# Kernel optimization log

Measured on AMD Instinct MI355X. Metric: run time of the kernel, lower is better.

The kernel has to match this reference:

```python
import jax, jax.numpy as jnp
import numpy as np

N_ITERS = 5
STRICT_MAXIMA_BONUS = 10.0
MAX_SUBPIXEL_SHIFT = 0.6


def setup_inputs() -> dict:
    key = jax.random.key(0)
    return {"x": jax.random.normal(key, (2, 4, 8, 256, 256), dtype=jnp.float32)}


def _nms3d_mask(x):
    # Strict 3x3x3 maxima: x > max over the 26 neighbors, replicate padding
    # (matches kornia nms3d(input, (3,3,3), mask_only=True)).
    B, C, D, H, W = x.shape
    p = jnp.pad(x, ((0, 0), (0, 0), (1, 1), (1, 1), (1, 1)), mode='edge')
    neigh_max = None
    for dd in range(3):
        for dh in range(3):
            for dw in range(3):
                if dd == 1 and dh == 1 and dw == 1:
                    continue
                s = p[:, :, dd:dd + D, dh:dh + H, dw:dw + W]
                neigh_max = s if neigh_max is None else jnp.maximum(neigh_max, s)
    return x > neigh_max


def _solve_cramer_sym3x3(dxx, dyy, dss, dxy, dxs, dys, r0, r1, r2):
    cf00 = dyy * dss - dys * dys
    cf01 = dxy * dss - dys * dxs
    cf02 = dxy * dys - dyy * dxs
    det = dxx * cf00 - dxy * cf01 + dxs * cf02
    solved = jnp.abs(det) > 0.0
    safe_det = jnp.where(solved, det, jnp.ones_like(det))
    sx = (r0 * cf00 - dxy * (r1 * dss - dys * r2) + dxs * (r1 * dys - dyy * r2)) / safe_det
    sy = (dxx * (r1 * dss - dys * r2) - r0 * cf01 + dxs * (dxy * r2 - r1 * dxs)) / safe_det
    ss = (dxx * (dyy * r2 - r1 * dys) - dxy * (dxy * r2 - r1 * dxs) + r0 * cf02) / safe_det
    return sx, sy, ss, solved


def _iterative_quad_interp3d(x, n_iters, strict_maxima_bonus, max_subpixel_shift):
    B, C, D, H, W = x.shape
    dtype = x.dtype
    BC = B * C
    HW = H * W
    DHW = D * HW
    i32 = jnp.int32

    # default grid coordinates, channel order [scale, x, y] as in the torch code
    gd = jnp.broadcast_to(jnp.arange(D, dtype=dtype)[:, None, None], (D, H, W))
    gw = jnp.broadcast_to(jnp.arange(W, dtype=dtype)[None, None, :], (D, H, W))
    gh = jnp.broadcast_to(jnp.arange(H, dtype=dtype)[None, :, None], (D, H, W))
    coords0 = jnp.broadcast_to(jnp.stack([gd, gw, gh], 0)[None, None], (B, C, 3, D, H, W))

    if D < 3 or H < 3 or W < 3:
        return coords0, x

    mask = _nms3d_mask(x)                       # (B,C,D,H,W) strict NMS maxima
    inp = x.reshape(BC, D, H, W)
    flat = inp.reshape(-1)
    m = mask.reshape(BC, D, H, W)

    # dense per-voxel formulation: every voxel runs the keypoint loop; only
    # voxels under the NMS mask are written out at the end (identical math,
    # since each keypoint's iteration depends only on its own patch chain).
    d0 = jnp.broadcast_to(jnp.arange(D, dtype=i32)[None, :, None, None], (BC, D, H, W))
    h0 = jnp.broadcast_to(jnp.arange(H, dtype=i32)[None, None, :, None], (BC, D, H, W))
    w0 = jnp.broadcast_to(jnp.arange(W, dtype=i32)[None, None, None, :], (BC, D, H, W))
    bc_base = (jnp.arange(BC, dtype=i32) * DHW)[:, None, None, None]

    d_cur, h_cur, w_cur = d0, h0, w0
    valid = jnp.ones((BC, D, H, W), dtype=bool)
    zeros = jnp.zeros((BC, D, H, W), dtype=dtype)
    shift_x, shift_y, shift_s, gds = zeros, zeros, zeros, zeros

    for _ in range(n_iters):
        d_s = jnp.clip(d_cur, 1, D - 2)
        h_s = jnp.clip(h_cur, 1, H - 2)
        w_s = jnp.clip(w_cur, 1, W - 2)
        base = bc_base + d_s * HW + h_s * W + w_s

        def tap(od, oh, ow):
            return jnp.take(flat, base + (od * HW + oh * W + ow))

        c000 = tap(0, 0, 0)
        p_xm = tap(0, 0, -1); p_xp = tap(0, 0, 1)
        p_ym = tap(0, -1, 0); p_yp = tap(0, 1, 0)
        p_sm = tap(-1, 0, 0); p_sp = tap(1, 0, 0)

        gx = 0.5 * (p_xp - p_xm)
        gy = 0.5 * (p_yp - p_ym)
        gs = 0.5 * (p_sp - p_sm)
        dxx = p_xp - 2.0 * c000 + p_xm
        dyy = p_yp - 2.0 * c000 + p_ym
        dss = p_sp - 2.0 * c000 + p_sm
        dxy = 0.25 * (tap(0, 1, 1) - tap(0, 1, -1) - tap(0, -1, 1) + tap(0, -1, -1))
        dxs = 0.25 * (tap(1, 0, 1) - tap(1, 0, -1) - tap(-1, 0, 1) + tap(-1, 0, -1))
        dys = 0.25 * (tap(1, 1, 0) - tap(1, -1, 0) - tap(-1, 1, 0) + tap(-1, -1, 0))

        sx, sy, ss, solved = _solve_cramer_sym3x3(dxx, dyy, dss, dxy, dxs, dys, -gx, -gy, -gs)
        valid = valid & solved
        vf = valid.astype(dtype)
        sx = sx * vf; sy = sy * vf; ss = ss * vf
        shift_x = jnp.where(valid, sx, shift_x)
        shift_y = jnp.where(valid, sy, shift_y)
        shift_s = jnp.where(valid, ss, shift_s)
        gds = jnp.where(valid, gx * sx + gy * sy + gs * ss, gds)

        # data-dependent recentering, sequentially per axis (x -> y -> scale)
        mv = (valid & (sx > max_subpixel_shift)).astype(i32) - (valid & (sx < -max_subpixel_shift)).astype(i32)
        new_w = w_cur + mv
        valid = valid & (new_w >= 1) & (new_w <= W - 2)
        w_cur = jnp.clip(new_w, 0, W - 1)

        mv = (valid & (sy > max_subpixel_shift)).astype(i32) - (valid & (sy < -max_subpixel_shift)).astype(i32)
        new_h = h_cur + mv
        valid = valid & (new_h >= 1) & (new_h <= H - 2)
        h_cur = jnp.clip(new_h, 0, H - 1)

        mv = (valid & (ss > max_subpixel_shift)).astype(i32) - (valid & (ss < -max_subpixel_shift)).astype(i32)
        new_d = d_cur + mv
        valid = valid & (new_d >= 1) & (new_d <= D - 2)
        d_cur = jnp.clip(new_d, 0, D - 1)

    valid = valid & (jnp.abs(shift_x) <= 1.5) & (jnp.abs(shift_y) <= 1.5) & (jnp.abs(shift_s) <= 1.5)

    final_s = jnp.where(valid, d_cur.astype(dtype) + shift_s, d0.astype(dtype))
    final_x = jnp.where(valid, w_cur.astype(dtype) + shift_x, w0.astype(dtype))
    final_y = jnp.where(valid, h_cur.astype(dtype) + shift_y, h0.astype(dtype))
    finals = jnp.stack([final_s, final_x, final_y], 1).reshape(B, C, 3, D, H, W)
    coords_max = jnp.where(mask[:, :, None], finals, coords0)

    corr = 0.5 * jnp.where(valid, gds, zeros)
    if strict_maxima_bonus > 0:
        corr = corr + strict_maxima_bonus * valid.astype(dtype)
    y_max = jnp.where(m, inp + corr, inp).reshape(B, C, D, H, W)
    return coords_max, y_max


def reference(x):
    return _iterative_quad_interp3d(x, N_ITERS, STRICT_MAXIMA_BONUS, MAX_SUBPIXEL_SHIFT)
```

## Files before the change

### kernel.cpp

```cpp
#include <hip/hip_runtime.h>

#define WD 256
#define HT 256
#define DP 8
#define NBC 8
#define HW 65536
#define DHW 524288
#define NVOX 4194304

__device__ void refine_write(const float* __restrict__ x,
                             float* __restrict__ out,
                             int idx) {
#pragma clang fp contract(off)
    const int w0 = idx & 255;
    const int h0 = (idx >> 8) & 255;
    const int d0 = (idx >> 16) & 7;
    const int bc = idx >> 19;
    int d = d0, h = h0, w = w0;
    bool valid = true;
    float shx = 0.f, shy = 0.f, shs = 0.f, gds = 0.f;
    const float* xb = x + (size_t)bc * DHW;
    for (int it = 0; it < 5; ++it) {
        int dcl = min(max(d, 1), DP - 2);
        int hcl = min(max(h, 1), HT - 2);
        int wcl = min(max(w, 1), WD - 2);
        const float* q = xb + dcl * HW + hcl * WD + wcl;
        float c000 = q[0];
        float pxm = q[-1],   pxp = q[1];
        float pym = q[-WD],  pyp = q[WD];
        float psm = q[-HW],  psp = q[HW];
        float gx = 0.5f * (pxp - pxm);
        float gy = 0.5f * (pyp - pym);
        float gs = 0.5f * (psp - psm);
        float dxx = pxp - 2.0f * c000 + pxm;
        float dyy = pyp - 2.0f * c000 + pym;
        float dss = psp - 2.0f * c000 + psm;
        float dxy = 0.25f * (q[WD + 1]  - q[WD - 1]  - q[-WD + 1]  + q[-WD - 1]);
        float dxs = 0.25f * (q[HW + 1]  - q[HW - 1]  - q[-HW + 1]  + q[-HW - 1]);
        float dys = 0.25f * (q[HW + WD] - q[HW - WD] - q[-HW + WD] + q[-HW - WD]);
        float r0 = -gx, r1 = -gy, r2 = -gs;
        float cf00 = dyy * dss - dys * dys;
        float cf01 = dxy * dss - dys * dxs;
        float cf02 = dxy * dys - dyy * dxs;
        float det = dxx * cf00 - dxy * cf01 + dxs * cf02;
        bool solved = fabsf(det) > 0.0f;
        float sdet = solved ? det : 1.0f;
        float sx = (r0 * cf00 - dxy * (r1 * dss - dys * r2) + dxs * (r1 * dys - dyy * r2)) / sdet;
        float sy = (dxx * (r1 * dss - dys * r2) - r0 * cf01 + dxs * (dxy * r2 - r1 * dxs)) / sdet;
        float ss = (dxx * (dyy * r2 - r1 * dys) - dxy * (dxy * r2 - r1 * dxs) + r0 * cf02) / sdet;
        valid = valid && solved;
        if (valid) {
            shx = sx; shy = sy; shs = ss;
            gds = gx * sx + gy * sy + gs * ss;
        } else {
            sx = 0.f; sy = 0.f; ss = 0.f;
        }
        int mvx = (valid && sx > 0.6f) ? 1 : ((valid && sx < -0.6f) ? -1 : 0);
        int nw = w + mvx;
        valid = valid && (nw >= 1) && (nw <= WD - 2);
        w = min(max(nw, 0), WD - 1);
        int mvy = (valid && sy > 0.6f) ? 1 : ((valid && sy < -0.6f) ? -1 : 0);
        int nh = h + mvy;
        valid = valid && (nh >= 1) && (nh <= HT - 2);
        h = min(max(nh, 0), HT - 1);
        int mvd = (valid && ss > 0.6f) ? 1 : ((valid && ss < -0.6f) ? -1 : 0);
        int nd = d + mvd;
        valid = valid && (nd >= 1) && (nd <= DP - 2);
        d = min(max(nd, 0), DP - 1);
        if (!valid) break;
        if (mvx == 0 && mvy == 0 && mvd == 0)
            break;
    }
    valid = valid && (fabsf(shx) <= 1.5f) && (fabsf(shy) <= 1.5f) && (fabsf(shs) <= 1.5f);
    if (!valid) return;

    size_t pos = (size_t)d0 * HW + (size_t)h0 * WD + (size_t)w0;
    float* cb = out + (size_t)(bc * 3) * DHW + pos;
    cb[0]         = (float)d + shs;
    cb[DHW]       = (float)w + shx;
    cb[2 * DHW]   = (float)h + shy;
    float corr = 0.5f * gds + 10.0f;
    float* yb = out + (size_t)NBC * 3 * DHW;
    yb[(size_t)bc * DHW + pos] = x[idx] + corr;
}

__global__ __launch_bounds__(256) void fused(const float* __restrict__ x,
                                             float* __restrict__ out) {
    int t = blockIdx.x * 256 + threadIdx.x;
    int lane = t & 63;
    int w0 = lane << 2;
    int h  = (t >> 6) & 255;
    int d  = (t >> 14) & 7;
    int bc = t >> 17;
    size_t pos = (size_t)d * HW + (size_t)h * WD + (size_t)w0;
    const float* xb = x + (size_t)bc * DHW;
    float4 c = *(const float4*)(xb + pos);

    float* yb = out + (size_t)NBC * 3 * DHW;
    *(float4*)(yb + (size_t)bc * DHW + pos) = c;
    float* cb = out + (size_t)(bc * 3) * DHW + pos;
    float fd = (float)d, fh = (float)h, fw = (float)w0;
    *(float4*)(cb)           = make_float4(fd, fd, fd, fd);
    *(float4*)(cb + DHW)     = make_float4(fw, fw + 1.f, fw + 2.f, fw + 3.f);
    *(float4*)(cb + 2 * DHW) = make_float4(fh, fh, fh, fh);

    if (d == 0 || d == DP - 1 || h == 0 || h == HT - 1) return;

    const float NEG = -3.4e38f;
    float n0 = NEG, n1 = NEG, n2 = NEG, n3 = NEG;
    const float* rowc = xb + pos;
#pragma unroll
    for (int dd = -1; dd <= 1; ++dd) {
#pragma unroll
        for (int hh = -1; hh <= 1; ++hh) {
            float4 v;
            if (dd == 0 && hh == 0) v = c;
            else v = *(const float4*)(rowc + dd * HW + hh * WD);
            float L = __shfl_up(v.w, 1);
            float R = __shfl_down(v.x, 1);
            if (dd == 0 && hh == 0) {
                n0 = fmaxf(n0, fmaxf(L,   v.y));
                n1 = fmaxf(n1, fmaxf(v.x, v.z));
                n2 = fmaxf(n2, fmaxf(v.y, v.w));
                n3 = fmaxf(n3, fmaxf(v.z, R));
            } else {
                n0 = fmaxf(n0, fmaxf(fmaxf(L,   v.x), v.y));
                n1 = fmaxf(n1, fmaxf(fmaxf(v.x, v.y), v.z));
                n2 = fmaxf(n2, fmaxf(fmaxf(v.y, v.z), v.w));
                n3 = fmaxf(n3, fmaxf(fmaxf(v.z, v.w), R));
            }
        }
    }
    bool m0 = (c.x > n0) && (w0 > 0);
    bool m1 = (c.y > n1);
    bool m2 = (c.z > n2);
    bool m3 = (c.w > n3) && (w0 + 3 < WD - 1);
    unsigned mbits = (m0 ? 1u : 0u) | (m1 ? 2u : 0u) | (m2 ? 4u : 0u) | (m3 ? 8u : 0u);
    if (!mbits) return;
    int vidx = (bc << 19) | (d << 16) | (h << 8) | w0;
    while (mbits) {
        int i = __ffs(mbits) - 1;
        mbits &= mbits - 1;
        refine_write(x, out, vidx + i);
    }
}

extern "C" void kernel_launch(void* const* d_in, const int* in_sizes, int n_in,
                              void* d_out, int out_size, void* d_ws, size_t ws_size,
                              hipStream_t stream) {
    const float* x = (const float*)d_in[0];
    float* out = (float*)d_out;
    (void)d_ws; (void)ws_size;
    fused<<<NVOX / 4 / 256, 256, 0, stream>>>(x, out);
}
```

Measured before the change: 90.84 us.

## Split NMS and refinement into two kernels with per-wave compacted maxima lists

Separates the fused kernel into an NMS pass that writes defaults and compacts each wave's maxima indices into a workspace list using ballot/popcount prefix sums, and a second kernel that refines one maximum per thread. This targets the divergence of the fused version, where only a few lanes per wave run the long serial refinement loop while the rest sit idle. In exchange it adds a second launch, workspace writes and reads, and a refine grid of about two million threads that mostly exit after reading a count. The old fused path stays as a fallback when the workspace is too small.

```diff
diff --git a/kernel.cpp b/kernel.cpp
--- a/kernel.cpp
+++ b/kernel.cpp
@@ -7,6 +7,8 @@
 #define HW 65536
 #define DHW 524288
 #define NVOX 4194304
+#define NWAVE 16384
+#define SLOTS 128
 
 __device__ void refine_write(const float* __restrict__ x,
                              float* __restrict__ out,
@@ -84,9 +86,9 @@
     yb[(size_t)bc * DHW + pos] = x[idx] + corr;
 }
 
-__global__ __launch_bounds__(256) void fused(const float* __restrict__ x,
-                                             float* __restrict__ out) {
-    int t = blockIdx.x * 256 + threadIdx.x;
+__device__ __forceinline__ int nms_defaults(const float* __restrict__ x,
+                                            float* __restrict__ out,
+                                            int t, unsigned* mbits_out) {
     int lane = t & 63;
     int w0 = lane << 2;
     int h  = (t >> 6) & 255;
@@ -104,7 +106,7 @@
     *(float4*)(cb + DHW)     = make_float4(fw, fw + 1.f, fw + 2.f, fw + 3.f);
     *(float4*)(cb + 2 * DHW) = make_float4(fh, fh, fh, fh);
 
-    if (d == 0 || d == DP - 1 || h == 0 || h == HT - 1) return;
+    if (d == 0 || d == DP - 1 || h == 0 || h == HT - 1) return -1;
 
     const float NEG = -3.4e38f;
     float n0 = NEG, n1 = NEG, n2 = NEG, n3 = NEG;
@@ -135,9 +137,57 @@
     bool m1 = (c.y > n1);
     bool m2 = (c.z > n2);
     bool m3 = (c.w > n3) && (w0 + 3 < WD - 1);
-    unsigned mbits = (m0 ? 1u : 0u) | (m1 ? 2u : 0u) | (m2 ? 4u : 0u) | (m3 ? 8u : 0u);
-    if (!mbits) return;
-    int vidx = (bc << 19) | (d << 16) | (h << 8) | w0;
+    *mbits_out = (m0 ? 1u : 0u) | (m1 ? 2u : 0u) | (m2 ? 4u : 0u) | (m3 ? 8u : 0u);
+    return (bc << 19) | (d << 16) | (h << 8) | w0;
+}
+
+__global__ __launch_bounds__(256) void nms_compact(const float* __restrict__ x,
+                                                   float* __restrict__ out,
+                                                   int* __restrict__ cnt,
+                                                   int* __restrict__ list) {
+    int t = blockIdx.x * 256 + threadIdx.x;
+    int lane = t & 63;
+    int wid = t >> 6;
+    unsigned mbits = 0;
+    int vidx = nms_defaults(x, out, t, &mbits);
+    if (vidx < 0) {
+        if (lane == 0) cnt[wid] = 0;
+        return;
+    }
+    unsigned long long lt = (lane == 0) ? 0ull : (~0ull >> (64 - lane));
+    unsigned long long b0 = __ballot(mbits & 1u);
+    unsigned long long b1 = __ballot(mbits & 2u);
+    unsigned long long b2 = __ballot(mbits & 4u);
+    unsigned long long b3 = __ballot(mbits & 8u);
+    int prefix = __popcll(b0 & lt) + __popcll(b1 & lt) +
+                 __popcll(b2 & lt) + __popcll(b3 & lt);
+    int total  = __popcll(b0) + __popcll(b1) + __popcll(b2) + __popcll(b3);
+    if (lane == 0) cnt[wid] = total;
+    int base = wid * SLOTS + prefix;
+    while (mbits) {
+        int i = __ffs(mbits) - 1;
+        mbits &= mbits - 1;
+        list[base++] = vidx + i;
+    }
+}
+
+__global__ __launch_bounds__(256) void refine_list(const float* __restrict__ x,
+                                                   float* __restrict__ out,
+                                                   const int* __restrict__ cnt,
+                                                   const int* __restrict__ list) {
+    int i = blockIdx.x * 256 + threadIdx.x;
+    int wid = i >> 7;
+    int slot = i & (SLOTS - 1);
+    if (slot < cnt[wid])
+        refine_write(x, out, list[wid * SLOTS + slot]);
+}
+
+__global__ __launch_bounds__(256) void fused(const float* __restrict__ x,
+                                             float* __restrict__ out) {
+    int t = blockIdx.x * 256 + threadIdx.x;
+    unsigned mbits = 0;
+    int vidx = nms_defaults(x, out, t, &mbits);
+    if (vidx < 0) return;
     while (mbits) {
         int i = __ffs(mbits) - 1;
         mbits &= mbits - 1;
@@ -150,6 +200,13 @@
                               hipStream_t stream) {
     const float* x = (const float*)d_in[0];
     float* out = (float*)d_out;
-    (void)d_ws; (void)ws_size;
-    fused<<<NVOX / 4 / 256, 256, 0, stream>>>(x, out);
-}
+    const size_t need = (size_t)NWAVE * 4 + (size_t)NWAVE * SLOTS * 4;
+    if (ws_size >= need) {
+        int* cnt  = (int*)d_ws;
+        int* list = (int*)((char*)d_ws + (size_t)NWAVE * 4);
+        nms_compact<<<NVOX / 4 / 256, 256, 0, stream>>>(x, out, cnt, list);
+        refine_list<<<NWAVE * SLOTS / 256, 256, 0, stream>>>(x, out, cnt, list);
+    } else {
+        fused<<<NVOX / 4 / 256, 256, 0, stream>>>(x, out);
+    }
+}
```

After: 99.50 us. 9.5% more time.

## Reuse NMS neighbourhood registers for first refinement step and merge output stores

Applied to the files above, without the earlier changes.

The first quadratic-fit iteration for each local maximum now takes its stencil values from the 3x3 row vectors already loaded for NMS, using shuffles, instead of issuing scattered global loads. Later iterations fall back to global loads only when the point moves. Default and refined outputs are merged in registers and written once with nontemporal float4 stores, which removes the scattered scalar overwrite stores. Launch bounds now request 4 blocks per SM, and the larger register set kept live could add pressure.

```diff
diff --git a/kernel.cpp b/kernel.cpp
--- a/kernel.cpp
+++ b/kernel.cpp
@@ -8,27 +8,45 @@
 #define DHW 524288
 #define NVOX 4194304
 
-__device__ void refine_write(const float* __restrict__ x,
-                             float* __restrict__ out,
-                             int idx) {
+typedef float f32x4 __attribute__((ext_vector_type(4)));
+
+__device__ __forceinline__ f32x4 ld4(const float* p) { return *(const f32x4*)p; }
+__device__ __forceinline__ void st4_nt(float* p, f32x4 v) {
+    __builtin_nontemporal_store(v, (f32x4*)p);
+}
+
+__device__ __forceinline__ bool solve3(float dxx, float dyy, float dss,
+                                       float dxy, float dxs, float dys,
+                                       float gx, float gy, float gs,
+                                       float& sx, float& sy, float& ss) {
 #pragma clang fp contract(off)
-    const int w0 = idx & 255;
-    const int h0 = (idx >> 8) & 255;
-    const int d0 = (idx >> 16) & 7;
-    const int bc = idx >> 19;
-    int d = d0, h = h0, w = w0;
+    float r0 = -gx, r1 = -gy, r2 = -gs;
+    float cf00 = dyy * dss - dys * dys;
+    float cf01 = dxy * dss - dys * dxs;
+    float cf02 = dxy * dys - dyy * dxs;
+    float det = dxx * cf00 - dxy * cf01 + dxs * cf02;
+    bool solved = fabsf(det) > 0.0f;
+    float sdet = solved ? det : 1.0f;
+    sx = (r0 * cf00 - dxy * (r1 * dss - dys * r2) + dxs * (r1 * dys - dyy * r2)) / sdet;
+    sy = (dxx * (r1 * dss - dys * r2) - r0 * cf01 + dxs * (dxy * r2 - r1 * dxs)) / sdet;
+    ss = (dxx * (dyy * r2 - r1 * dys) - dxy * (dxy * r2 - r1 * dxs) + r0 * cf02) / sdet;
+    return solved;
+}
+
+__device__ bool refine_cont(const float* __restrict__ xb,
+                            int& d, int& h, int& w,
+                            float& shx, float& shy, float& shs, float& gds) {
+#pragma clang fp contract(off)
     bool valid = true;
-    float shx = 0.f, shy = 0.f, shs = 0.f, gds = 0.f;
-    const float* xb = x + (size_t)bc * DHW;
-    for (int it = 0; it < 5; ++it) {
+    for (int it = 1; it < 5; ++it) {
         int dcl = min(max(d, 1), DP - 2);
         int hcl = min(max(h, 1), HT - 2);
         int wcl = min(max(w, 1), WD - 2);
         const float* q = xb + dcl * HW + hcl * WD + wcl;
         float c000 = q[0];
-        float pxm = q[-1],   pxp = q[1];
-        float pym = q[-WD],  pyp = q[WD];
-        float psm = q[-HW],  psp = q[HW];
+        float pxm = q[-1],  pxp = q[1];
+        float pym = q[-WD], pyp = q[WD];
+        float psm = q[-HW], psp = q[HW];
         float gx = 0.5f * (pxp - pxm);
         float gy = 0.5f * (pyp - pym);
         float gs = 0.5f * (psp - psm);
@@ -38,16 +56,8 @@
         float dxy = 0.25f * (q[WD + 1]  - q[WD - 1]  - q[-WD + 1]  + q[-WD - 1]);
         float dxs = 0.25f * (q[HW + 1]  - q[HW - 1]  - q[-HW + 1]  + q[-HW - 1]);
         float dys = 0.25f * (q[HW + WD] - q[HW - WD] - q[-HW + WD] + q[-HW - WD]);
-        float r0 = -gx, r1 = -gy, r2 = -gs;
-        float cf00 = dyy * dss - dys * dys;
-        float cf01 = dxy * dss - dys * dxs;
-        float cf02 = dxy * dys - dyy * dxs;
-        float det = dxx * cf00 - dxy * cf01 + dxs * cf02;
-        bool solved = fabsf(det) > 0.0f;
-        float sdet = solved ? det : 1.0f;
-        float sx = (r0 * cf00 - dxy * (r1 * dss - dys * r2) + dxs * (r1 * dys - dyy * r2)) / sdet;
-        float sy = (dxx * (r1 * dss - dys * r2) - r0 * cf01 + dxs * (dxy * r2 - r1 * dxs)) / sdet;
-        float ss = (dxx * (dyy * r2 - r1 * dys) - dxy * (dxy * r2 - r1 * dxs) + r0 * cf02) / sdet;
+        float sx, sy, ss;
+        bool solved = solve3(dxx, dyy, dss, dxy, dxs, dys, gx, gy, gs, sx, sy, ss);
         valid = valid && solved;
         if (valid) {
             shx = sx; shy = sy; shs = ss;
@@ -68,24 +78,14 @@
         valid = valid && (nd >= 1) && (nd <= DP - 2);
         d = min(max(nd, 0), DP - 1);
         if (!valid) break;
-        if (mvx == 0 && mvy == 0 && mvd == 0)
-            break;
+        if (mvx == 0 && mvy == 0 && mvd == 0) break;
     }
-    valid = valid && (fabsf(shx) <= 1.5f) && (fabsf(shy) <= 1.5f) && (fabsf(shs) <= 1.5f);
-    if (!valid) return;
-
-    size_t pos = (size_t)d0 * HW + (size_t)h0 * WD + (size_t)w0;
-    float* cb = out + (size_t)(bc * 3) * DHW + pos;
-    cb[0]         = (float)d + shs;
-    cb[DHW]       = (float)w + shx;
-    cb[2 * DHW]   = (float)h + shy;
-    float corr = 0.5f * gds + 10.0f;
-    float* yb = out + (size_t)NBC * 3 * DHW;
-    yb[(size_t)bc * DHW + pos] = x[idx] + corr;
-}
-
-__global__ __launch_bounds__(256) void fused(const float* __restrict__ x,
-                                             float* __restrict__ out) {
+    return valid && (fabsf(shx) <= 1.5f) && (fabsf(shy) <= 1.5f) && (fabsf(shs) <= 1.5f);
+}
+
+__global__ __launch_bounds__(256, 4) void fused(const float* __restrict__ x,
+                                                float* __restrict__ out) {
+#pragma clang fp contract(off)
     int t = blockIdx.x * 256 + threadIdx.x;
     int lane = t & 63;
     int w0 = lane << 2;
@@ -94,55 +94,135 @@
     int bc = t >> 17;
     size_t pos = (size_t)d * HW + (size_t)h * WD + (size_t)w0;
     const float* xb = x + (size_t)bc * DHW;
-    float4 c = *(const float4*)(xb + pos);
-
-    float* yb = out + (size_t)NBC * 3 * DHW;
-    *(float4*)(yb + (size_t)bc * DHW + pos) = c;
+    const float* rowc = xb + pos;
+    f32x4 c = ld4(rowc);
+
+    float fd = (float)d, fh = (float)h, fw = (float)w0;
+    float* yb = out + (size_t)NBC * 3 * DHW + (size_t)bc * DHW + pos;
     float* cb = out + (size_t)(bc * 3) * DHW + pos;
-    float fd = (float)d, fh = (float)h, fw = (float)w0;
-    *(float4*)(cb)           = make_float4(fd, fd, fd, fd);
-    *(float4*)(cb + DHW)     = make_float4(fw, fw + 1.f, fw + 2.f, fw + 3.f);
-    *(float4*)(cb + 2 * DHW) = make_float4(fh, fh, fh, fh);
-
-    if (d == 0 || d == DP - 1 || h == 0 || h == HT - 1) return;
+    f32x4 ocs = {fd, fd, fd, fd};
+    f32x4 ocx = {fw, fw + 1.f, fw + 2.f, fw + 3.f};
+    f32x4 ocy = {fh, fh, fh, fh};
+    f32x4 oy  = c;
+
+    if (d == 0 || d == DP - 1 || h == 0 || h == HT - 1) {
+        st4_nt(cb, ocs); st4_nt(cb + DHW, ocx); st4_nt(cb + 2 * DHW, ocy); st4_nt(yb, oy);
+        return;
+    }
+
+    f32x4 rmm = ld4(rowc - HW - WD);
+    f32x4 rm0 = ld4(rowc - HW);
+    f32x4 rmp = ld4(rowc - HW + WD);
+    f32x4 r0m = ld4(rowc - WD);
+    f32x4 r00 = c;
+    f32x4 r0p = ld4(rowc + WD);
+    f32x4 rpm = ld4(rowc + HW - WD);
+    f32x4 rp0 = ld4(rowc + HW);
+    f32x4 rpp = ld4(rowc + HW + WD);
+
+    float Lmm = __shfl_up(rmm.w, 1), Rmm = __shfl_down(rmm.x, 1);
+    float Lm0 = __shfl_up(rm0.w, 1), Rm0 = __shfl_down(rm0.x, 1);
+    float Lmp = __shfl_up(rmp.w, 1), Rmp = __shfl_down(rmp.x, 1);
+    float L0m = __shfl_up(r0m.w, 1), R0m = __shfl_down(r0m.x, 1);
+    float L00 = __shfl_up(r00.w, 1), R00 = __shfl_down(r00.x, 1);
+    float L0p = __shfl_up(r0p.w, 1), R0p = __shfl_down(r0p.x, 1);
+    float Lpm = __shfl_up(rpm.w, 1), Rpm = __shfl_down(rpm.x, 1);
+    float Lp0 = __shfl_up(rp0.w, 1), Rp0 = __shfl_down(rp0.x, 1);
+    float Lpp = __shfl_up(rpp.w, 1), Rpp = __shfl_down(rpp.x, 1);
 
     const float NEG = -3.4e38f;
     float n0 = NEG, n1 = NEG, n2 = NEG, n3 = NEG;
-    const float* rowc = xb + pos;
-#pragma unroll
-    for (int dd = -1; dd <= 1; ++dd) {
-#pragma unroll
-        for (int hh = -1; hh <= 1; ++hh) {
-            float4 v;
-            if (dd == 0 && hh == 0) v = c;
-            else v = *(const float4*)(rowc + dd * HW + hh * WD);
-            float L = __shfl_up(v.w, 1);
-            float R = __shfl_down(v.x, 1);
-            if (dd == 0 && hh == 0) {
-                n0 = fmaxf(n0, fmaxf(L,   v.y));
-                n1 = fmaxf(n1, fmaxf(v.x, v.z));
-                n2 = fmaxf(n2, fmaxf(v.y, v.w));
-                n3 = fmaxf(n3, fmaxf(v.z, R));
-            } else {
-                n0 = fmaxf(n0, fmaxf(fmaxf(L,   v.x), v.y));
-                n1 = fmaxf(n1, fmaxf(fmaxf(v.x, v.y), v.z));
-                n2 = fmaxf(n2, fmaxf(fmaxf(v.y, v.z), v.w));
-                n3 = fmaxf(n3, fmaxf(fmaxf(v.z, v.w), R));
-            }
-        }
-    }
+#define ACC(vv, LL, RR)                                  \
+    n0 = fmaxf(n0, fmaxf(fmaxf(LL, vv.x), vv.y));        \
+    n1 = fmaxf(n1, fmaxf(fmaxf(vv.x, vv.y), vv.z));      \
+    n2 = fmaxf(n2, fmaxf(fmaxf(vv.y, vv.z), vv.w));      \
+    n3 = fmaxf(n3, fmaxf(fmaxf(vv.z, vv.w), RR));
+    ACC(rmm, Lmm, Rmm) ACC(rm0, Lm0, Rm0) ACC(rmp, Lmp, Rmp)
+    ACC(r0m, L0m, R0m)                    ACC(r0p, L0p, R0p)
+    ACC(rpm, Lpm, Rpm) ACC(rp0, Lp0, Rp0) ACC(rpp, Lpp, Rpp)
+#undef ACC
+    n0 = fmaxf(n0, fmaxf(L00,   r00.y));
+    n1 = fmaxf(n1, fmaxf(r00.x, r00.z));
+    n2 = fmaxf(n2, fmaxf(r00.y, r00.w));
+    n3 = fmaxf(n3, fmaxf(r00.z, R00));
+
     bool m0 = (c.x > n0) && (w0 > 0);
     bool m1 = (c.y > n1);
     bool m2 = (c.z > n2);
     bool m3 = (c.w > n3) && (w0 + 3 < WD - 1);
     unsigned mbits = (m0 ? 1u : 0u) | (m1 ? 2u : 0u) | (m2 ? 4u : 0u) | (m3 ? 8u : 0u);
-    if (!mbits) return;
-    int vidx = (bc << 19) | (d << 16) | (h << 8) | w0;
-    while (mbits) {
-        int i = __ffs(mbits) - 1;
-        mbits &= mbits - 1;
-        refine_write(x, out, vidx + i);
+
+    if (mbits) {
+#define SEL3(row, LL, RR, am1, a0, ap1)                                          \
+        am1 = (i == 0) ? LL    : ((i == 1) ? row.x : ((i == 2) ? row.y : row.z)); \
+        a0  = (i == 0) ? row.x : ((i == 1) ? row.y : ((i == 2) ? row.z : row.w)); \
+        ap1 = (i == 0) ? row.y : ((i == 1) ? row.z : ((i == 2) ? row.w : RR));
+#define SEL0(row) ((i == 0) ? row.x : ((i == 1) ? row.y : ((i == 2) ? row.z : row.w)))
+        unsigned mb = mbits;
+        while (mb) {
+            int i = __ffs(mb) - 1;
+            mb &= mb - 1;
+            float pxm, c000, pxp;          SEL3(r00, L00, R00, pxm, c000, pxp);
+            float ym_m1, ym_0, ym_p1;      SEL3(r0m, L0m, R0m, ym_m1, ym_0, ym_p1);
+            float yp_m1, yp_0, yp_p1;      SEL3(r0p, L0p, R0p, yp_m1, yp_0, yp_p1);
+            float sm_m1, sm_0, sm_p1;      SEL3(rm0, Lm0, Rm0, sm_m1, sm_0, sm_p1);
+            float sp_m1, sp_0, sp_p1;      SEL3(rp0, Lp0, Rp0, sp_m1, sp_0, sp_p1);
+            float gx = 0.5f * (pxp - pxm);
+            float gy = 0.5f * (yp_0 - ym_0);
+            float gs = 0.5f * (sp_0 - sm_0);
+            float dxx = pxp - 2.0f * c000 + pxm;
+            float dyy = yp_0 - 2.0f * c000 + ym_0;
+            float dss = sp_0 - 2.0f * c000 + sm_0;
+            float dxy = 0.25f * (yp_p1 - yp_m1 - ym_p1 + ym_m1);
+            float dxs = 0.25f * (sp_p1 - sp_m1 - sm_p1 + sm_m1);
+            float dys = 0.25f * (SEL0(rpp) - SEL0(rpm) - SEL0(rmp) + SEL0(rmm));
+            float sx, sy, ss;
+            bool valid = solve3(dxx, dyy, dss, dxy, dxs, dys, gx, gy, gs, sx, sy, ss);
+            if (valid) {
+                float shx = sx, shy = sy, shs = ss;
+                float gds = gx * sx + gy * sy + gs * ss;
+                int w = w0 + i, hh = h, dd = d;
+                int mvx = (sx > 0.6f) ? 1 : ((sx < -0.6f) ? -1 : 0);
+                int nw = w + mvx;
+                bool v2 = (nw >= 1) && (nw <= WD - 2);
+                w = min(max(nw, 0), WD - 1);
+                int mvy = v2 ? ((sy > 0.6f) ? 1 : ((sy < -0.6f) ? -1 : 0)) : 0;
+                int nh = hh + mvy;
+                v2 = v2 && (nh >= 1) && (nh <= HT - 2);
+                hh = min(max(nh, 0), HT - 1);
+                int mvd = v2 ? ((ss > 0.6f) ? 1 : ((ss < -0.6f) ? -1 : 0)) : 0;
+                int nd = dd + mvd;
+                v2 = v2 && (nd >= 1) && (nd <= DP - 2);
+                dd = min(max(nd, 0), DP - 1);
+                bool wr = false;
+                float fs = 0.f, fx = 0.f, fy = 0.f, yv = 0.f;
+                if (v2) {
+                    if (mvx == 0 && mvy == 0 && mvd == 0) {
+                        wr = true;
+                        fs = (float)dd + shs; fx = (float)w + shx; fy = (float)hh + shy;
+                        yv = c000 + 0.5f * gds + 10.0f;
+                    } else {
+                        bool ok = refine_cont(xb, dd, hh, w, shx, shy, shs, gds);
+                        if (ok) {
+                            wr = true;
+                            fs = (float)dd + shs; fx = (float)w + shx; fy = (float)hh + shy;
+                            yv = c000 + 0.5f * gds + 10.0f;
+                        }
+                    }
+                }
+                if (wr) {
+                    if      (i == 0) { ocs.x = fs; ocx.x = fx; ocy.x = fy; oy.x = yv; }
+                    else if (i == 1) { ocs.y = fs; ocx.y = fx; ocy.y = fy; oy.y = yv; }
+                    else if (i == 2) { ocs.z = fs; ocx.z = fx; ocy.z = fy; oy.z = yv; }
+                    else             { ocs.w = fs; ocx.w = fx; ocy.w = fy; oy.w = yv; }
+                }
+            }
+        }
+#undef SEL3
+#undef SEL0
     }
+
+    st4_nt(cb, ocs); st4_nt(cb + DHW, ocx); st4_nt(cb + 2 * DHW, ocy); st4_nt(yb, oy);
 }
 
 extern "C" void kernel_launch(void* const* d_in, const int* in_sizes, int n_in,
```

New measurement: 102.6 us. +12.9%, slower.

## Process four rows per wave with sliding window reuse of neighbor rows

Applied to the files above, without the earlier changes.

Each wavefront now handles four consecutive H rows of one depth slice. The 3x3 neighbor rows are kept in registers and slid along H, so each step loads three new rows instead of nine. The refinement routine is marked noinline so its register use stays out of the main loop. The grid shrinks to 1024 blocks, which lowers parallelism and occupancy and serializes the four rows within each wave.

```diff
diff --git a/kernel.cpp b/kernel.cpp
--- a/kernel.cpp
+++ b/kernel.cpp
@@ -8,9 +8,9 @@
 #define DHW 524288
 #define NVOX 4194304
 
-__device__ void refine_write(const float* __restrict__ x,
-                             float* __restrict__ out,
-                             int idx) {
+__device__ __attribute__((noinline)) void refine_write(const float* __restrict__ x,
+                                                       float* __restrict__ out,
+                                                       int idx) {
 #pragma clang fp contract(off)
     const int w0 = idx & 255;
     const int h0 = (idx >> 8) & 255;
@@ -84,64 +84,117 @@
     yb[(size_t)bc * DHW + pos] = x[idx] + corr;
 }
 
-__global__ __launch_bounds__(256) void fused(const float* __restrict__ x,
-                                             float* __restrict__ out) {
-    int t = blockIdx.x * 256 + threadIdx.x;
-    int lane = t & 63;
-    int w0 = lane << 2;
-    int h  = (t >> 6) & 255;
-    int d  = (t >> 14) & 7;
-    int bc = t >> 17;
+struct Row { float4 v; float L, R; };
+
+__device__ __forceinline__ Row load_row(const float* __restrict__ xb,
+                                        int dd, int hh, int w0) {
+    Row r;
+    r.v = *(const float4*)(xb + (size_t)dd * HW + (size_t)hh * WD + w0);
+    r.L = __shfl_up(r.v.w, 1);
+    r.R = __shfl_down(r.v.x, 1);
+    return r;
+}
+
+__device__ __forceinline__ void write_defaults(float* __restrict__ out,
+                                               int bc, int d, int h, int w0,
+                                               float4 c) {
     size_t pos = (size_t)d * HW + (size_t)h * WD + (size_t)w0;
-    const float* xb = x + (size_t)bc * DHW;
-    float4 c = *(const float4*)(xb + pos);
-
-    float* yb = out + (size_t)NBC * 3 * DHW;
-    *(float4*)(yb + (size_t)bc * DHW + pos) = c;
+    float* yb = out + (size_t)NBC * 3 * DHW + (size_t)bc * DHW + pos;
+    *(float4*)yb = c;
     float* cb = out + (size_t)(bc * 3) * DHW + pos;
     float fd = (float)d, fh = (float)h, fw = (float)w0;
     *(float4*)(cb)           = make_float4(fd, fd, fd, fd);
     *(float4*)(cb + DHW)     = make_float4(fw, fw + 1.f, fw + 2.f, fw + 3.f);
     *(float4*)(cb + 2 * DHW) = make_float4(fh, fh, fh, fh);
-
-    if (d == 0 || d == DP - 1 || h == 0 || h == HT - 1) return;
-
+}
+
+__global__ __launch_bounds__(256) void fused(const float* __restrict__ x,
+                                             float* __restrict__ out) {
+    int lane = threadIdx.x & 63;
+    int wib  = threadIdx.x >> 6;
+    int g    = blockIdx.x * 4 + wib;
+    int q    = g & 63;
+    int slab = g >> 6;
+    int d    = slab & 7;
+    int bc   = slab >> 3;
+    int w0   = lane << 2;
+    const float* xb = x + (size_t)bc * DHW;
+    int hbase = q << 2;
+
+    if (d == 0 || d == DP - 1) {
+#pragma unroll
+        for (int k = 0; k < 4; ++k) {
+            int h = hbase + k;
+            float4 c = *(const float4*)(xb + (size_t)d * HW + (size_t)h * WD + w0);
+            write_defaults(out, bc, d, h, w0, c);
+        }
+        return;
+    }
+
+    Row pm, p0, pp, cm, c0, cp, nm, n0, np;
+    bool primed = false;
     const float NEG = -3.4e38f;
-    float n0 = NEG, n1 = NEG, n2 = NEG, n3 = NEG;
-    const float* rowc = xb + pos;
+
 #pragma unroll
-    for (int dd = -1; dd <= 1; ++dd) {
-#pragma unroll
-        for (int hh = -1; hh <= 1; ++hh) {
-            float4 v;
-            if (dd == 0 && hh == 0) v = c;
-            else v = *(const float4*)(rowc + dd * HW + hh * WD);
-            float L = __shfl_up(v.w, 1);
-            float R = __shfl_down(v.x, 1);
-            if (dd == 0 && hh == 0) {
-                n0 = fmaxf(n0, fmaxf(L,   v.y));
-                n1 = fmaxf(n1, fmaxf(v.x, v.z));
-                n2 = fmaxf(n2, fmaxf(v.y, v.w));
-                n3 = fmaxf(n3, fmaxf(v.z, R));
-            } else {
-                n0 = fmaxf(n0, fmaxf(fmaxf(L,   v.x), v.y));
-                n1 = fmaxf(n1, fmaxf(fmaxf(v.x, v.y), v.z));
-                n2 = fmaxf(n2, fmaxf(fmaxf(v.y, v.z), v.w));
-                n3 = fmaxf(n3, fmaxf(fmaxf(v.z, v.w), R));
+    for (int k = 0; k < 4; ++k) {
+        int h = hbase + k;
+        if (h == 0) {
+            float4 c = *(const float4*)(xb + (size_t)h * WD + w0 + (size_t)d * HW);
+            write_defaults(out, bc, d, h, w0, c);
+            continue;
+        }
+        if (h == HT - 1) {
+            write_defaults(out, bc, d, h, w0, n0.v);
+            continue;
+        }
+        if (!primed) {
+            pm = load_row(xb, d - 1, h - 1, w0);
+            p0 = load_row(xb, d,     h - 1, w0);
+            pp = load_row(xb, d + 1, h - 1, w0);
+            cm = load_row(xb, d - 1, h,     w0);
+            c0 = load_row(xb, d,     h,     w0);
+            cp = load_row(xb, d + 1, h,     w0);
+            nm = load_row(xb, d - 1, h + 1, w0);
+            n0 = load_row(xb, d,     h + 1, w0);
+            np = load_row(xb, d + 1, h + 1, w0);
+            primed = true;
+        } else {
+            pm = cm; p0 = c0; pp = cp;
+            cm = nm; c0 = n0; cp = np;
+            nm = load_row(xb, d - 1, h + 1, w0);
+            n0 = load_row(xb, d,     h + 1, w0);
+            np = load_row(xb, d + 1, h + 1, w0);
+        }
+        write_defaults(out, bc, d, h, w0, c0.v);
+
+        float n0m = NEG, n1m = NEG, n2m = NEG, n3m = NEG;
+#define ACC(rr)                                                    \
+        n0m = fmaxf(n0m, fmaxf(fmaxf(rr.L,   rr.v.x), rr.v.y));    \
+        n1m = fmaxf(n1m, fmaxf(fmaxf(rr.v.x, rr.v.y), rr.v.z));    \
+        n2m = fmaxf(n2m, fmaxf(fmaxf(rr.v.y, rr.v.z), rr.v.w));    \
+        n3m = fmaxf(n3m, fmaxf(fmaxf(rr.v.z, rr.v.w), rr.R));
+        ACC(pm) ACC(p0) ACC(pp)
+        ACC(cm)         ACC(cp)
+        ACC(nm) ACC(n0) ACC(np)
+#undef ACC
+        n0m = fmaxf(n0m, fmaxf(c0.L,   c0.v.y));
+        n1m = fmaxf(n1m, fmaxf(c0.v.x, c0.v.z));
+        n2m = fmaxf(n2m, fmaxf(c0.v.y, c0.v.w));
+        n3m = fmaxf(n3m, fmaxf(c0.v.z, c0.R));
+
+        bool m0 = (c0.v.x > n0m) && (w0 > 0);
+        bool m1 = (c0.v.y > n1m);
+        bool m2 = (c0.v.z > n2m);
+        bool m3 = (c0.v.w > n3m) && (w0 + 3 < WD - 1);
+        unsigned mbits = (m0 ? 1u : 0u) | (m1 ? 2u : 0u) | (m2 ? 4u : 0u) | (m3 ? 8u : 0u);
+        if (mbits) {
+            int vidx = (bc << 19) | (d << 16) | (h << 8) | w0;
+            while (mbits) {
+                int i = __ffs(mbits) - 1;
+                mbits &= mbits - 1;
+                refine_write(x, out, vidx + i);
             }
         }
-    }
-    bool m0 = (c.x > n0) && (w0 > 0);
-    bool m1 = (c.y > n1);
-    bool m2 = (c.z > n2);
-    bool m3 = (c.w > n3) && (w0 + 3 < WD - 1);
-    unsigned mbits = (m0 ? 1u : 0u) | (m1 ? 2u : 0u) | (m2 ? 4u : 0u) | (m3 ? 8u : 0u);
-    if (!mbits) return;
-    int vidx = (bc << 19) | (d << 16) | (h << 8) | w0;
-    while (mbits) {
-        int i = __ffs(mbits) - 1;
-        mbits &= mbits - 1;
-        refine_write(x, out, vidx + i);
     }
 }
 
@@ -151,5 +204,5 @@
     const float* x = (const float*)d_in[0];
     float* out = (float*)d_out;
     (void)d_ws; (void)ws_size;
-    fused<<<NVOX / 4 / 256, 256, 0, stream>>>(x, out);
-}
+    fused<<<1024, 256, 0, stream>>>(x, out);
+}
```

New measurement: 95.45 us. +5.1%, slower.
